# Optimization experiments

Hardware: AMD Instinct MI355X
Metric: run time of the kernel (lower is better)

The kernel has to match this reference:

```python
import jax, jax.numpy as jnp
import numpy as np

B, S, H = 4, 2048, 1024
NH, HD = 16, 64
ROPE_THETA = 160000.0
SCALE = HD ** -0.5


def _rope_cos_sin(position_ids, dim, theta):
    # neox-style rotary: frequencies over half the head dim
    inv_freq = 1.0 / (theta ** (jnp.arange(0, dim, 2, dtype=jnp.float32) / dim))  # [dim/2]
    freqs = position_ids.astype(jnp.float32)[..., None] * inv_freq  # [B,S,dim/2]
    return jnp.cos(freqs), jnp.sin(freqs)


def _apply_rope(x, cos, sin):
    # x: [B,S,NH,HD]; neox style: rotate halves
    d2 = x.shape[-1] // 2
    x1, x2 = x[..., :d2], x[..., d2:]
    c = cos[:, :, None, :]
    s = sin[:, :, None, :]
    return jnp.concatenate([x1 * c - x2 * s, x2 * c + x1 * s], axis=-1)


def setup_inputs() -> dict:
    key = jax.random.key(0)
    k1, k2, k3 = jax.random.split(key, 3)
    hidden_states = jax.random.normal(k1, (B, S, H), dtype=jnp.float32)
    position_ids = jnp.tile(jnp.arange(S, dtype=jnp.int32)[None, :], (B, 1))
    Wqkv = jax.random.normal(k2, (3 * H, H), dtype=jnp.float32) * (H ** -0.5)
    Wo = jax.random.normal(k3, (H, H), dtype=jnp.float32) * (H ** -0.5)
    return {"hidden_states": hidden_states, "position_ids": position_ids,
            "Wqkv": Wqkv, "Wo": Wo}


def reference(hidden_states, position_ids, Wqkv, Wo):
    # fused QKV projection
    qkv = jnp.einsum('bsh,oh->bso', hidden_states, Wqkv)  # [B,S,3H]
    q, k, v = jnp.split(qkv, 3, axis=-1)
    q = q.reshape(B, S, NH, HD)
    k = k.reshape(B, S, NH, HD)
    v = v.reshape(B, S, NH, HD)
    # rotary embedding (neox style)
    cos, sin = _rope_cos_sin(position_ids, HD, ROPE_THETA)
    q = _apply_rope(q, cos, sin)
    k = _apply_rope(k, cos, sin)
    # full bidirectional (encoder-only, global layer) attention
    scores = jnp.einsum('bqhd,bkhd->bhqk', q, k) * SCALE  # [B,NH,S,S]
    probs = jax.nn.softmax(scores, axis=-1)
    ctx = jnp.einsum('bhqk,bkhd->bqhd', probs, v).reshape(B, S, H)
    # output projection
    return jnp.einsum('bsh,oh->bso', ctx, Wo)
```

## Files before the change

### kernel.cpp

```cpp
#include <hip/hip_runtime.h>
#include <hip/hip_bf16.h>


#define GLOBAL_AS __attribute__((address_space(1)))
#define LDS_AS    __attribute__((address_space(3)))

using f32x4 = __attribute__((ext_vector_type(4))) float;
using s16x8 = __attribute__((ext_vector_type(8))) short;

__device__ __forceinline__ void gld_lds16(const void* g, void* l) {
  __builtin_amdgcn_global_load_lds((const GLOBAL_AS void*)g, (LDS_AS void*)l, 16, 0, 0);
}

__device__ __forceinline__ unsigned short f2bf(float f) {
  unsigned int u = __float_as_uint(f);
  u = (u + 0x7fffu + ((u >> 16) & 1u)) >> 16;
  return (unsigned short)u;
}
__device__ __forceinline__ unsigned int cvt_pk_bf16(float lo, float hi) {
  unsigned int r;
  asm("v_cvt_pk_bf16_f32 %0, %1, %2" : "=v"(r) : "v"(lo), "v"(hi));
  return r;
}

__global__ __launch_bounds__(256) void cvt_bf16_kernel(const float* __restrict__ src,
                                                       unsigned short* __restrict__ dst) {
  int i = blockIdx.x * 256 + threadIdx.x;
  float4 v = ((const float4*)src)[i];
  ushort4 o;
  o.x = f2bf(v.x); o.y = f2bf(v.y); o.z = f2bf(v.z); o.w = f2bf(v.w);
  ((ushort4*)dst)[i] = o;
}

__global__ __launch_bounds__(256) void rope_table_kernel(const int* __restrict__ pos,
                                                         float* __restrict__ ctab,
                                                         float* __restrict__ stab) {
  int idx = blockIdx.x * 256 + threadIdx.x;
  int d = idx & 31;
  int bs = idx >> 5;
  float p = (float)pos[bs];
  float inv = exp2f(-(float)d * 0.5402410118609203f);
  float f = p * inv;
  ctab[idx] = cosf(f);
  stab[idx] = sinf(f);
}

template<int MODE>
__global__ __launch_bounds__(256) void gemm_bt_kernel(const unsigned short* __restrict__ A,
                                                      const unsigned short* __restrict__ Bm,
                                                      void* __restrict__ C, int N, int K,
                                                      const float* __restrict__ ctab,
                                                      const float* __restrict__ stab,
                                                      unsigned short* __restrict__ Qr,
                                                      unsigned short* __restrict__ Kr,
                                                      unsigned short* __restrict__ vbuf) {
  __shared__ char sA[16384];
  __shared__ char sB[16384];
  const int tid  = threadIdx.x;
  const int lane = tid & 63, w = tid >> 6;
  const int g = lane >> 4, c = lane & 15;
  const int wr = w >> 1, wc = w & 1;
  const int m0 = blockIdx.x * 128, n0 = blockIdx.y * 128;
  const char* Ab = (const char*)A;
  const char* Bb = (const char*)Bm;

  f32x4 acc[4][4] = {};
  for (int k0 = 0; k0 < K; k0 += 64) {
    __syncthreads();
#pragma unroll
    for (int rr = 0; rr < 4; ++rr) {
      int o = tid * 16 + rr * 4096;
      int row = o >> 7;
      int col = (o & 127) ^ ((row & 7) << 4);
      gld_lds16(Ab + ((size_t)(m0 + row) * K + k0) * 2 + col, sA + o);
      gld_lds16(Bb + ((size_t)(n0 + row) * K + k0) * 2 + col, sB + o);
    }
    __syncthreads();
#pragma unroll
    for (int ks = 0; ks < 2; ++ks) {
      s16x8 af[4], bfr[4];
#pragma unroll
      for (int i = 0; i < 4; ++i) {
        int row = 64 * wr + 16 * i + c;
        af[i] = *(const s16x8*)(sA + ((row * 128 + ks * 64 + g * 16) ^ ((row & 7) << 4)));
      }
#pragma unroll
      for (int j = 0; j < 4; ++j) {
        int row = 64 * wc + 16 * j + c;
        bfr[j] = *(const s16x8*)(sB + ((row * 128 + ks * 64 + g * 16) ^ ((row & 7) << 4)));
      }
#pragma unroll
      for (int i = 0; i < 4; ++i)
#pragma unroll
        for (int j = 0; j < 4; ++j)
          acc[i][j] = __builtin_amdgcn_mfma_f32_16x16x32_bf16(af[i], bfr[j], acc[i][j], 0, 0, 0);
    }
  }

  if (MODE == 1) {
#pragma unroll
    for (int i = 0; i < 4; ++i)
#pragma unroll
      for (int j = 0; j < 4; ++j)
#pragma unroll
        for (int r = 0; r < 4; ++r) {
          int m = m0 + 64 * wr + 16 * i + 4 * g + r;
          int n = n0 + 64 * wc + 16 * j + c;
          ((float*)C)[(size_t)m * N + n] = acc[i][j][r];
        }
  } else {
    const int t = blockIdx.y;
    if (t < 16) {
      unsigned short* dstb = (t < 8) ? Qr : Kr;
      const float qs = (t < 8) ? 0.18033688011112042f : 1.0f;
      const int h = 2 * (t & 7) + wc;
#pragma unroll
      for (int i = 0; i < 4; ++i)
#pragma unroll
        for (int r = 0; r < 4; ++r) {
          int m = m0 + 64 * wr + 16 * i + 4 * g + r;
          int b = m >> 11, s = m & 2047;
          unsigned short* drow = dstb + ((size_t)(b * 16 + h) * 2048 + s) * 64;
#pragma unroll
          for (int j = 0; j < 2; ++j) {
            int d = 16 * j + c;
            float co = ctab[(size_t)m * 32 + d];
            float si = stab[(size_t)m * 32 + d];
            float x1 = acc[i][j][r], x2 = acc[i][j + 2][r];
            drow[d]      = f2bf((x1 * co - x2 * si) * qs);
            drow[d + 32] = f2bf((x2 * co + x1 * si) * qs);
          }
        }
    } else {
#pragma unroll
      for (int i = 0; i < 4; ++i)
#pragma unroll
        for (int j = 0; j < 4; ++j)
#pragma unroll
          for (int r = 0; r < 4; ++r) {
            int m = m0 + 64 * wr + 16 * i + 4 * g + r;
            int n = (t - 16) * 128 + 64 * wc + 16 * j + c;
            vbuf[(size_t)m * 1024 + n] = f2bf(acc[i][j][r]);
          }
    }
  }
}

__global__ __launch_bounds__(256) void vtrans_kernel(const unsigned short* __restrict__ vbuf,
                                                     unsigned short* __restrict__ Vt) {
  __shared__ unsigned short tile[64][80];
  int bid = blockIdx.x;
  int st = bid & 31, h = (bid >> 5) & 15, b = bid >> 9;
  int s0 = st * 64;
  int t = threadIdx.x;
  {
    int row = t >> 2, part = t & 3;
    const unsigned short* src = vbuf + ((size_t)(b * 2048 + s0 + row)) * 1024 + h * 64 + part * 16;
    uint4 v0 = *(const uint4*)(src);
    uint4 v1 = *(const uint4*)(src + 8);
    *(uint4*)&tile[row][part * 16]     = v0;
    *(uint4*)&tile[row][part * 16 + 8] = v1;
  }
  __syncthreads();
  {
    int d = t >> 2, sp = t & 3;
    unsigned short vals[16];
#pragma unroll
    for (int i = 0; i < 16; ++i) vals[i] = tile[sp * 16 + i][d];
    unsigned short* dst = Vt + ((size_t)(b * 16 + h) * 64 + d) * 2048 + s0 + sp * 16;
    *(uint4*)(dst)     = ((const uint4*)vals)[0];
    *(uint4*)(dst + 8) = ((const uint4*)vals)[1];
  }
}

__global__ __launch_bounds__(256, 3) void attn_kernel(const unsigned short* __restrict__ Q,
                                                      const unsigned short* __restrict__ Kr,
                                                      const unsigned short* __restrict__ Vt,
                                                      unsigned short* __restrict__ Ctx) {
  __shared__ char sK[2][8192];
  __shared__ char sV[2][8192];
  __shared__ char sP[16384];
  const int tid  = threadIdx.x;
  const int lane = tid & 63, w = tid >> 6;
  const int g = lane >> 4, c = lane & 15;
  const int bh = blockIdx.x;
  const int q0 = blockIdx.y * 128;
  const char* kh = (const char*)(Kr + (size_t)bh * 2048 * 64);
  const char* vh = (const char*)(Vt + (size_t)bh * 64 * 2048);

  s16x8 qf[2][2];
#pragma unroll
  for (int u = 0; u < 2; ++u) {
    const char* qrow = (const char*)(Q + (size_t)bh * 2048 * 64) + (size_t)(q0 + 32 * w + 16 * u + c) * 128;
    qf[u][0] = *(const s16x8*)(qrow + g * 16);
    qf[u][1] = *(const s16x8*)(qrow + 64 + g * 16);
  }

#pragma unroll
  for (int rr = 0; rr < 2; ++rr) {
    int o = tid * 16 + rr * 4096;
    int l = o ^ (((o >> 7) & 7) << 4);
    gld_lds16(kh + l, sK[0] + o);
    gld_lds16(vh + (size_t)(o >> 7) * 4096 + (l & 127), sV[0] + o);
  }

  float l_run[2] = {0.f, 0.f};
  f32x4 o_acc[2][4] = {};
  char* pw0 = sP + w * 4096;
  char* pw1 = pw0 + 2048;

  for (int it = 0; it < 32; ++it) {
    __syncthreads();
    const int cur = it & 1;
    if (it + 1 < 32) {
      int kvn = (it + 1) * 64;
#pragma unroll
      for (int rr = 0; rr < 2; ++rr) {
        int o = tid * 16 + rr * 4096;
        int l = o ^ (((o >> 7) & 7) << 4);
        gld_lds16(kh + (size_t)kvn * 128 + l, sK[cur ^ 1] + o);
        gld_lds16(vh + (size_t)(o >> 7) * 4096 + kvn * 2 + (l & 127), sV[cur ^ 1] + o);
      }
    }

    f32x4 sc[2][4] = {};
#pragma unroll
    for (int j = 0; j < 4; ++j) {
      int row = 16 * j + c;
#pragma unroll
      for (int ks = 0; ks < 2; ++ks) {
        s16x8 kb = *(const s16x8*)(sK[cur] + ((row * 128 + ks * 64 + g * 16) ^ ((c & 7) << 4)));
        sc[0][j] = __builtin_amdgcn_mfma_f32_16x16x32_bf16(kb, qf[0][ks], sc[0][j], 0, 0, 0);
        sc[1][j] = __builtin_amdgcn_mfma_f32_16x16x32_bf16(kb, qf[1][ks], sc[1][j], 0, 0, 0);
      }
    }

#pragma unroll
    for (int u = 0; u < 2; ++u) {
      char* pw = u ? pw1 : pw0;
      float rs = 0.f;
#pragma unroll
      for (int j = 0; j < 4; ++j) {
        float e0 = __builtin_amdgcn_exp2f(sc[u][j][0]);
        float e1 = __builtin_amdgcn_exp2f(sc[u][j][1]);
        float e2 = __builtin_amdgcn_exp2f(sc[u][j][2]);
        float e3 = __builtin_amdgcn_exp2f(sc[u][j][3]);
        rs += (e0 + e1) + (e2 + e3);
        uint2 pk;
        pk.x = cvt_pk_bf16(e0, e1);
        pk.y = cvt_pk_bf16(e2, e3);
        *(uint2*)(pw + ((c * 128 + 32 * j + 8 * g) ^ ((c & 7) << 4))) = pk;
      }
      l_run[u] += rs;
    }
    asm volatile("s_waitcnt lgkmcnt(0)" ::: "memory");

#pragma unroll
    for (int ns = 0; ns < 2; ++ns) {
      s16x8 pa0 = *(const s16x8*)(pw0 + ((c * 128 + ns * 64 + g * 16) ^ ((c & 7) << 4)));
      s16x8 pa1 = *(const s16x8*)(pw1 + ((c * 128 + ns * 64 + g * 16) ^ ((c & 7) << 4)));
#pragma unroll
      for (int dj = 0; dj < 4; ++dj) {
        int row = 16 * dj + c;
        s16x8 vb = *(const s16x8*)(sV[cur] + ((row * 128 + ns * 64 + g * 16) ^ ((c & 7) << 4)));
        o_acc[0][dj] = __builtin_amdgcn_mfma_f32_16x16x32_bf16(pa0, vb, o_acc[0][dj], 0, 0, 0);
        o_acc[1][dj] = __builtin_amdgcn_mfma_f32_16x16x32_bf16(pa1, vb, o_acc[1][dj], 0, 0, 0);
      }
    }
  }

  const int b = bh >> 4, h = bh & 15;
#pragma unroll
  for (int u = 0; u < 2; ++u) {
    float l = l_run[u];
    l += __shfl_xor(l, 16);
    l += __shfl_xor(l, 32);
#pragma unroll
    for (int r = 0; r < 4; ++r) {
      float lr = __shfl(l, (lane & 48) | (4 * g + r));
      float inv = 1.f / lr;
      int srow = q0 + 32 * w + 16 * u + 4 * g + r;
      unsigned short* crow = Ctx + ((size_t)(b * 2048 + srow)) * 1024 + h * 64;
#pragma unroll
      for (int dj = 0; dj < 4; ++dj)
        crow[16 * dj + c] = f2bf(o_acc[u][dj][r] * inv);
    }
  }
}

extern "C" void kernel_launch(void* const* d_in, const int* in_sizes, int n_in,
                              void* d_out, int out_size, void* d_ws, size_t ws_size,
                              hipStream_t stream) {
  const float* hidden = (const float*)d_in[0];
  const int*   pos    = (const int*)d_in[1];
  const float* wqkv   = (const float*)d_in[2];
  const float* wo     = (const float*)d_in[3];

  char* ws = (char*)d_ws;
  unsigned short* hbf  = (unsigned short*)(ws);
  unsigned short* wqbf = (unsigned short*)(ws + 16777216);
  unsigned short* wobf = (unsigned short*)(ws + 23068672);
  unsigned short* vbuf = (unsigned short*)(ws + 25165824);
  unsigned short* Qr   = (unsigned short*)(ws + 41943040);
  unsigned short* Kr   = (unsigned short*)(ws + 58720256);
  unsigned short* Vt   = (unsigned short*)(ws + 75497472);
  unsigned short* ctx  = (unsigned short*)(ws + 92274688);
  float*          ctab = (float*)(ws + 109051904);
  float*          stab = (float*)(ws + 110100480);

  cvt_bf16_kernel<<<8192, 256, 0, stream>>>(hidden, hbf);
  cvt_bf16_kernel<<<3072, 256, 0, stream>>>(wqkv, wqbf);
  cvt_bf16_kernel<<<1024, 256, 0, stream>>>(wo, wobf);
  rope_table_kernel<<<1024, 256, 0, stream>>>(pos, ctab, stab);

  dim3 gq(64, 24);
  gemm_bt_kernel<2><<<gq, 256, 0, stream>>>(hbf, wqbf, nullptr, 3072, 1024,
                                            ctab, stab, Qr, Kr, vbuf);

  vtrans_kernel<<<2048, 256, 0, stream>>>(vbuf, Vt);

  dim3 ga(64, 16);
  attn_kernel<<<ga, 256, 0, stream>>>(Qr, Kr, Vt, ctx);

  dim3 go(64, 8);
  gemm_bt_kernel<1><<<go, 256, 0, stream>>>(ctx, wobf, d_out, 1024, 1024,
                                            nullptr, nullptr, nullptr, nullptr, nullptr);
}
```

Before: 210.4 us.

## Load K fragments straight to registers, split QK by half, remap attention blocks

The attention kernel no longer stages K through shared memory. Each lane loads its K fragments from global memory into registers and prefetches the next tile between the two half-tile QK^T passes. The QK/softmax work is split per 16-row half so exp of one half overlaps MFMA of the other, MFMA phases get s_setprio, and occupancy is raised to 4 blocks via lower LDS. Block indices are remapped so co-resident blocks share K/V heads for L2 reuse, and the three conversion kernels are fused into one launch. Risks include register pressure at 4 waves and exposed global latency on K loads.

```diff
diff --git a/kernel.cpp b/kernel.cpp
--- a/kernel.cpp
+++ b/kernel.cpp
@@ -23,9 +23,17 @@
   return r;
 }
 
-__global__ __launch_bounds__(256) void cvt_bf16_kernel(const float* __restrict__ src,
-                                                       unsigned short* __restrict__ dst) {
-  int i = blockIdx.x * 256 + threadIdx.x;
+__global__ __launch_bounds__(256) void cvt_all_kernel(const float* __restrict__ h,
+                                                      const float* __restrict__ wq,
+                                                      const float* __restrict__ wo,
+                                                      unsigned short* __restrict__ hb,
+                                                      unsigned short* __restrict__ wqb,
+                                                      unsigned short* __restrict__ wob) {
+  int b = blockIdx.x;
+  const float* src; unsigned short* dst; int i;
+  if (b < 8192)       { src = h;  dst = hb;  i = b * 256 + threadIdx.x; }
+  else if (b < 11264) { src = wq; dst = wqb; i = (b - 8192) * 256 + threadIdx.x; }
+  else                { src = wo; dst = wob; i = (b - 11264) * 256 + threadIdx.x; }
   float4 v = ((const float4*)src)[i];
   ushort4 o;
   o.x = f2bf(v.x); o.y = f2bf(v.y); o.z = f2bf(v.z); o.w = f2bf(v.w);
@@ -173,18 +181,19 @@
   }
 }
 
-__global__ __launch_bounds__(256, 3) void attn_kernel(const unsigned short* __restrict__ Q,
+__global__ __launch_bounds__(256, 4) void attn_kernel(const unsigned short* __restrict__ Q,
                                                       const unsigned short* __restrict__ Kr,
                                                       const unsigned short* __restrict__ Vt,
                                                       unsigned short* __restrict__ Ctx) {
-  __shared__ char sK[2][8192];
   __shared__ char sV[2][8192];
   __shared__ char sP[16384];
   const int tid  = threadIdx.x;
   const int lane = tid & 63, w = tid >> 6;
   const int g = lane >> 4, c = lane & 15;
-  const int bh = blockIdx.x;
-  const int q0 = blockIdx.y * 128;
+  int lin = blockIdx.x + 16 * blockIdx.y;
+  int eff = (lin & 7) * 128 + (lin >> 3);
+  const int bh = eff >> 4;
+  const int q0 = (eff & 15) * 128;
   const char* kh = (const char*)(Kr + (size_t)bh * 2048 * 64);
   const char* vh = (const char*)(Vt + (size_t)bh * 64 * 2048);
 
@@ -196,11 +205,18 @@
     qf[u][1] = *(const s16x8*)(qrow + 64 + g * 16);
   }
 
+  const char* kbase = kh + (size_t)c * 128 + g * 16;
+  s16x8 kreg[4][2];
+#pragma unroll
+  for (int j = 0; j < 4; ++j)
+#pragma unroll
+    for (int ks = 0; ks < 2; ++ks)
+      kreg[j][ks] = *(const s16x8*)(kbase + j * 2048 + ks * 64);
+
 #pragma unroll
   for (int rr = 0; rr < 2; ++rr) {
     int o = tid * 16 + rr * 4096;
     int l = o ^ (((o >> 7) & 7) << 4);
-    gld_lds16(kh + l, sK[0] + o);
     gld_lds16(vh + (size_t)(o >> 7) * 4096 + (l & 127), sV[0] + o);
   }
 
@@ -218,43 +234,72 @@
       for (int rr = 0; rr < 2; ++rr) {
         int o = tid * 16 + rr * 4096;
         int l = o ^ (((o >> 7) & 7) << 4);
-        gld_lds16(kh + (size_t)kvn * 128 + l, sK[cur ^ 1] + o);
         gld_lds16(vh + (size_t)(o >> 7) * 4096 + kvn * 2 + (l & 127), sV[cur ^ 1] + o);
       }
     }
 
-    f32x4 sc[2][4] = {};
-#pragma unroll
-    for (int j = 0; j < 4; ++j) {
-      int row = 16 * j + c;
-#pragma unroll
-      for (int ks = 0; ks < 2; ++ks) {
-        s16x8 kb = *(const s16x8*)(sK[cur] + ((row * 128 + ks * 64 + g * 16) ^ ((c & 7) << 4)));
-        sc[0][j] = __builtin_amdgcn_mfma_f32_16x16x32_bf16(kb, qf[0][ks], sc[0][j], 0, 0, 0);
-        sc[1][j] = __builtin_amdgcn_mfma_f32_16x16x32_bf16(kb, qf[1][ks], sc[1][j], 0, 0, 0);
-      }
-    }
-
-#pragma unroll
-    for (int u = 0; u < 2; ++u) {
-      char* pw = u ? pw1 : pw0;
+    __builtin_amdgcn_s_setprio(1);
+    f32x4 sc0[4] = {};
+#pragma unroll
+    for (int j = 0; j < 4; ++j)
+#pragma unroll
+      for (int ks = 0; ks < 2; ++ks)
+        sc0[j] = __builtin_amdgcn_mfma_f32_16x16x32_bf16(kreg[j][ks], qf[0][ks], sc0[j], 0, 0, 0);
+    __builtin_amdgcn_s_setprio(0);
+    {
       float rs = 0.f;
 #pragma unroll
       for (int j = 0; j < 4; ++j) {
-        float e0 = __builtin_amdgcn_exp2f(sc[u][j][0]);
-        float e1 = __builtin_amdgcn_exp2f(sc[u][j][1]);
-        float e2 = __builtin_amdgcn_exp2f(sc[u][j][2]);
-        float e3 = __builtin_amdgcn_exp2f(sc[u][j][3]);
+        float e0 = __builtin_amdgcn_exp2f(sc0[j][0]);
+        float e1 = __builtin_amdgcn_exp2f(sc0[j][1]);
+        float e2 = __builtin_amdgcn_exp2f(sc0[j][2]);
+        float e3 = __builtin_amdgcn_exp2f(sc0[j][3]);
         rs += (e0 + e1) + (e2 + e3);
         uint2 pk;
         pk.x = cvt_pk_bf16(e0, e1);
         pk.y = cvt_pk_bf16(e2, e3);
-        *(uint2*)(pw + ((c * 128 + 32 * j + 8 * g) ^ ((c & 7) << 4))) = pk;
-      }
-      l_run[u] += rs;
+        *(uint2*)(pw0 + ((c * 128 + 32 * j + 8 * g) ^ ((c & 7) << 4))) = pk;
+      }
+      l_run[0] += rs;
+    }
+
+    __builtin_amdgcn_s_setprio(1);
+    f32x4 sc1[4] = {};
+#pragma unroll
+    for (int j = 0; j < 4; ++j)
+#pragma unroll
+      for (int ks = 0; ks < 2; ++ks)
+        sc1[j] = __builtin_amdgcn_mfma_f32_16x16x32_bf16(kreg[j][ks], qf[1][ks], sc1[j], 0, 0, 0);
+    __builtin_amdgcn_s_setprio(0);
+
+    if (it + 1 < 32) {
+      const char* kb2 = kbase + (size_t)(it + 1) * 8192;
+#pragma unroll
+      for (int j = 0; j < 4; ++j)
+#pragma unroll
+        for (int ks = 0; ks < 2; ++ks)
+          kreg[j][ks] = *(const s16x8*)(kb2 + j * 2048 + ks * 64);
+    }
+
+    {
+      float rs = 0.f;
+#pragma unroll
+      for (int j = 0; j < 4; ++j) {
+        float e0 = __builtin_amdgcn_exp2f(sc1[j][0]);
+        float e1 = __builtin_amdgcn_exp2f(sc1[j][1]);
+        float e2 = __builtin_amdgcn_exp2f(sc1[j][2]);
+        float e3 = __builtin_amdgcn_exp2f(sc1[j][3]);
+        rs += (e0 + e1) + (e2 + e3);
+        uint2 pk;
+        pk.x = cvt_pk_bf16(e0, e1);
+        pk.y = cvt_pk_bf16(e2, e3);
+        *(uint2*)(pw1 + ((c * 128 + 32 * j + 8 * g) ^ ((c & 7) << 4))) = pk;
+      }
+      l_run[1] += rs;
     }
     asm volatile("s_waitcnt lgkmcnt(0)" ::: "memory");
 
+    __builtin_amdgcn_s_setprio(1);
 #pragma unroll
     for (int ns = 0; ns < 2; ++ns) {
       s16x8 pa0 = *(const s16x8*)(pw0 + ((c * 128 + ns * 64 + g * 16) ^ ((c & 7) << 4)));
@@ -267,6 +312,7 @@
         o_acc[1][dj] = __builtin_amdgcn_mfma_f32_16x16x32_bf16(pa1, vb, o_acc[1][dj], 0, 0, 0);
       }
     }
+    __builtin_amdgcn_s_setprio(0);
   }
 
   const int b = bh >> 4, h = bh & 15;
@@ -308,9 +354,7 @@
   float*          ctab = (float*)(ws + 109051904);
   float*          stab = (float*)(ws + 110100480);
 
-  cvt_bf16_kernel<<<8192, 256, 0, stream>>>(hidden, hbf);
-  cvt_bf16_kernel<<<3072, 256, 0, stream>>>(wqkv, wqbf);
-  cvt_bf16_kernel<<<1024, 256, 0, stream>>>(wo, wobf);
+  cvt_all_kernel<<<12288, 256, 0, stream>>>(hidden, wqkv, wo, hbf, wqbf, wobf);
   rope_table_kernel<<<1024, 256, 0, stream>>>(pos, ctab, stab);
 
   dim3 gq(64, 24);
@@ -319,7 +363,7 @@
 
   vtrans_kernel<<<2048, 256, 0, stream>>>(vbuf, Vt);
 
-  dim3 ga(64, 16);
+  dim3 ga(16, 64);
   attn_kernel<<<ga, 256, 0, stream>>>(Qr, Kr, Vt, ctx);
 
   dim3 go(64, 8);
```

After: 288.8 us. 37.2% more time.
